# Performance work log

Measured on AMD Instinct MI355X. Metric: run time of the kernel, lower is better.

Reference implementation:

```python
import jax, jax.numpy as jnp
import numpy as np

N = 51200      # total nodes
E = 1638400    # total edges (avg degree 32)
G = 512        # graphs in batch
IN = 16        # input node features
H = 4          # heads
C = 32         # channels per head
HC = H * C     # 128, concat output width
SLOPE = 0.2    # LeakyReLU negative slope
BN_EPS = 1e-5


def _glorot(k, shape, fan):
    return jax.random.normal(k, shape, jnp.float32) / np.sqrt(fan).astype(np.float32)


def setup_inputs() -> dict:
    key = jax.random.key(0)
    ks = jax.random.split(key, 32)
    inp = {}
    inp['x'] = jax.random.normal(ks[0], (N, IN), jnp.float32)
    inp['edge_index'] = jax.random.randint(ks[1], (2, E), 0, N)
    inp['batch'] = jnp.sort(jax.random.randint(ks[2], (N,), 0, G))
    # GATv2 layer 1 (IN -> H*C)
    inp['l1_Wl'] = _glorot(ks[3], (IN, HC), IN)
    inp['l1_bl'] = jnp.zeros((HC,), jnp.float32)
    inp['l1_Wr'] = _glorot(ks[4], (IN, HC), IN)
    inp['l1_br'] = jnp.zeros((HC,), jnp.float32)
    inp['l1_att'] = _glorot(ks[5], (H, C), C)
    inp['l1_bias'] = jnp.zeros((HC,), jnp.float32)
    # GATv2 layer 2 (HC -> H*C)
    inp['l2_Wl'] = _glorot(ks[6], (HC, HC), HC)
    inp['l2_bl'] = jnp.zeros((HC,), jnp.float32)
    inp['l2_Wr'] = _glorot(ks[7], (HC, HC), HC)
    inp['l2_br'] = jnp.zeros((HC,), jnp.float32)
    inp['l2_att'] = _glorot(ks[8], (H, C), C)
    inp['l2_bias'] = jnp.zeros((HC,), jnp.float32)
    # MLP head (HC -> HC -> HC -> 2) with BatchNorm (eval mode, running stats 0/1)
    inp['fc1_W'] = _glorot(ks[9], (HC, HC), HC)
    inp['fc1_b'] = jnp.zeros((HC,), jnp.float32)
    inp['bn1_g'] = jnp.ones((HC,), jnp.float32)
    inp['bn1_b'] = jnp.zeros((HC,), jnp.float32)
    inp['fc2_W'] = _glorot(ks[10], (HC, HC), HC)
    inp['fc2_b'] = jnp.zeros((HC,), jnp.float32)
    inp['bn2_g'] = jnp.ones((HC,), jnp.float32)
    inp['bn2_b'] = jnp.zeros((HC,), jnp.float32)
    inp['fc3_W'] = _glorot(ks[11], (HC, 2), HC)
    inp['fc3_b'] = jnp.zeros((2,), jnp.float32)
    return inp


def gatv2_conv(x, src, dst, Wl, bl, Wr, br, att, bias):
    # PyG GATv2Conv (share_weights=False, concat=True), eval mode (no dropout).
    xl = (x @ Wl + bl).reshape(-1, H, C)  # source transform  [N,H,C]
    xr = (x @ Wr + br).reshape(-1, H, C)  # target transform  [N,H,C]
    e = jax.nn.leaky_relu(xl[src] + xr[dst], SLOPE)   # [E,H,C]
    score = jnp.einsum('ehc,hc->eh', e, att)          # [E,H]
    # segment softmax over edges sharing the same target node
    m = jax.ops.segment_max(score, dst, num_segments=N)
    ex = jnp.exp(score - m[dst])
    denom = jax.ops.segment_sum(ex, dst, num_segments=N)
    alpha = ex / (denom[dst] + 1e-16)                 # [E,H]
    out = jax.ops.segment_sum(xl[src] * alpha[:, :, None], dst, num_segments=N)
    return out.reshape(-1, HC) + bias


def reference(x, edge_index, batch,
              l1_Wl, l1_bl, l1_Wr, l1_br, l1_att, l1_bias,
              l2_Wl, l2_bl, l2_Wr, l2_br, l2_att, l2_bias,
              fc1_W, fc1_b, bn1_g, bn1_b,
              fc2_W, fc2_b, bn2_g, bn2_b,
              fc3_W, fc3_b):
    src, dst = edge_index[0], edge_index[1]
    h = jax.nn.relu(gatv2_conv(x, src, dst, l1_Wl, l1_bl, l1_Wr, l1_br, l1_att, l1_bias))
    h = jax.nn.relu(gatv2_conv(h, src, dst, l2_Wl, l2_bl, l2_Wr, l2_br, l2_att, l2_bias))
    # global mean pool over graphs
    s = jax.ops.segment_sum(h, batch, num_segments=G)
    cnt = jax.ops.segment_sum(jnp.ones((N,), h.dtype), batch, num_segments=G)
    g = s / jnp.maximum(cnt, 1.0)[:, None]            # [G,HC]
    # MLP head; BatchNorm1d in eval mode with running_mean=0, running_var=1
    def bn(z, gamma, beta):
        return z * (gamma / np.sqrt(1.0 + BN_EPS).astype(np.float32)) + beta
    g = jax.nn.relu(bn(g @ fc1_W + fc1_b, bn1_g, bn1_b))
    g = jax.nn.relu(bn(g @ fc2_W + fc2_b, bn2_g, bn2_b))
    return g @ fc3_W + fc3_b                          # [G,2]
```

## Files before the change

kernel.cpp:

```cpp
#include <hip/hip_runtime.h>
#include <math.h>

#define NN 51200
#define EE 1638400
#define GG 512
#define INF 16
#define HCC 128
#define NB 400
#define TILE 4096
#define NBLK (NN / 4)

typedef float vf2 __attribute__((ext_vector_type(2)));
#define FMA2 __builtin_elementwise_fma
#define MIN2 __builtin_elementwise_min
#define MAX2 __builtin_elementwise_max


__device__ __forceinline__ int wave_incl_scan(int v, int lane) {
#pragma unroll
    for (int d = 1; d < 64; d <<= 1) {
        int y = __shfl_up(v, d);
        if (lane >= d) v += y;
    }
    return v;
}

__global__ __launch_bounds__(256) void k_hist(const int* __restrict__ ei,
                                              int* __restrict__ bcnt) {
    __shared__ int h[NB];
    for (int i = threadIdx.x; i < NB; i += 256) h[i] = 0;
    __syncthreads();
    int e0 = blockIdx.x * TILE;
#pragma unroll
    for (int s = 0; s < 16; s++) {
        int d = ei[EE + e0 + s * 256 + threadIdx.x];
        atomicAdd(&h[d >> 7], 1);
    }
    __syncthreads();
    for (int i = threadIdx.x; i < NB; i += 256)
        if (h[i]) atomicAdd(&bcnt[i], h[i]);
}

__global__ __launch_bounds__(512) void k_scan2(const int* __restrict__ bcnt,
                                               int* __restrict__ bbase,
                                               int* __restrict__ gcur,
                                               int* __restrict__ rowptr) {
    __shared__ int sc[512];
    int t = threadIdx.x;
    int v = (t < NB) ? bcnt[t] : 0;
    sc[t] = v;
    __syncthreads();
    for (int off = 1; off < 512; off <<= 1) {
        int u = (t >= off) ? sc[t - off] : 0;
        __syncthreads();
        sc[t] += u;
        __syncthreads();
    }
    if (t < NB) { int ex = sc[t] - v; bbase[t] = ex; gcur[t] = ex; }
    if (t == 0) { bbase[NB] = EE; rowptr[NN] = EE; }
}

__global__ __launch_bounds__(512) void k_bin(const int* __restrict__ ei,
                                             int* __restrict__ gcur,
                                             unsigned* __restrict__ binned) {
    __shared__ int h[512];
    __shared__ int lexcl[NB], lcur[NB], baseg[NB];
    __shared__ unsigned stage[TILE];
    __shared__ int wsum[8];
    int t = threadIdx.x;
    int lane = t & 63, w = t >> 6;
    h[t] = 0;
    __syncthreads();
    int e0 = blockIdx.x * TILE;
    int sv[8], dv[8];
#pragma unroll
    for (int s = 0; s < 8; s++) {
        int e = e0 + s * 512 + t;
        sv[s] = ei[e];
        dv[s] = ei[EE + e];
        atomicAdd(&h[dv[s] >> 7], 1);
    }
    __syncthreads();
    int myh = h[t];
    int incl = wave_incl_scan(myh, lane);
    if (lane == 63) wsum[w] = incl;
    __syncthreads();
    int woff = 0;
    for (int i = 0; i < w; i++) woff += wsum[i];
    incl += woff;
    if (t < NB) {
        int ex = incl - myh;
        lexcl[t] = ex;
        lcur[t] = ex;
        baseg[t] = atomicAdd(&gcur[t], myh);
    }
    __syncthreads();
#pragma unroll
    for (int s = 0; s < 8; s++) {
        int b = dv[s] >> 7;
        int r = atomicAdd(&lcur[b], 1);
        stage[r] = (unsigned)sv[s] | ((unsigned)dv[s] << 16);
    }
    __syncthreads();
#pragma unroll
    for (int s = 0; s < 8; s++) {
        int idx = s * 512 + t;
        unsigned p = stage[idx];
        int b = (int)(p >> 23);
        binned[baseg[b] + idx - lexcl[b]] = p;
    }
}

__global__ __launch_bounds__(256) void k_csr(const unsigned* __restrict__ binned,
                                             const int* __restrict__ bbase,
                                             int* __restrict__ rowptr,
                                             int* __restrict__ col) {
    int b = blockIdx.x;
    int base = bbase[b];
    int cnt = bbase[b + 1] - base;
    __shared__ int nh[1024], ncur[1024];
    __shared__ int wsum[4];
    int t = threadIdx.x;
    int lane = t & 63, w = t >> 6;
#pragma unroll
    for (int i = 0; i < 4; i++) nh[t + 256 * i] = 0;
    __syncthreads();
    for (int e = t; e < cnt; e += 256) {
        unsigned p = binned[base + e];
        unsigned src = p & 0xFFFFu;
        int key = (int)(((p >> 16) & 127u) << 3) | (int)(src >> 13);
        atomicAdd(&nh[key], 1);
    }
    __syncthreads();
    int c0 = nh[4 * t + 0], c1 = nh[4 * t + 1], c2 = nh[4 * t + 2], c3 = nh[4 * t + 3];
    int tot = ((c0 + c1) + (c2 + c3));
    int incl = wave_incl_scan(tot, lane);
    if (lane == 63) wsum[w] = incl;
    __syncthreads();
    int woff = 0;
    for (int i = 0; i < w; i++) woff += wsum[i];
    int tex = incl + woff - tot;
    ncur[4 * t + 0] = base + tex;
    ncur[4 * t + 1] = base + tex + c0;
    ncur[4 * t + 2] = base + tex + c0 + c1;
    ncur[4 * t + 3] = base + tex + c0 + c1 + c2;
    if ((t & 1) == 0) rowptr[(b << 7) + (t >> 1)] = base + tex;
    __syncthreads();
    for (int e = t; e < cnt; e += 256) {
        unsigned p = binned[base + e];
        unsigned src = p & 0xFFFFu;
        int key = (int)(((p >> 16) & 127u) << 3) | (int)(src >> 13);
        int r = atomicAdd(&ncur[key], 1);
        col[r] = (int)src;
    }
}

__global__ __launch_bounds__(256) void k_lin1(const float* __restrict__ x,
                                              const float* __restrict__ Wl,
                                              const float* __restrict__ bl,
                                              const float* __restrict__ Wr,
                                              const float* __restrict__ br,
                                              float* __restrict__ xl,
                                              float* __restrict__ xr) {
    __shared__ float sx[2][INF];
    int j = threadIdx.x & 127;
    int ty = threadIdx.x >> 7;
    int row = blockIdx.x * 2 + ty;
    if (threadIdx.x < 32) {
        int r = blockIdx.x * 2 + (threadIdx.x >> 4);
        sx[threadIdx.x >> 4][threadIdx.x & 15] = x[(size_t)r * INF + (threadIdx.x & 15)];
    }
    __syncthreads();
    float al = bl[j], ar = br[j];
#pragma unroll
    for (int k = 0; k < INF; k++) {
        float xv = sx[ty][k];
        al = fmaf(xv, Wl[k * HCC + j], al);
        ar = fmaf(xv, Wr[k * HCC + j], ar);
    }
    size_t s = ((size_t)(j >> 5) * NN + row) * 32 + (j & 31);
    xl[s] = al;
    xr[s] = ar;
}

#define AST 129
#define BST 260
__global__ __launch_bounds__(512) void k_lin2(const float* __restrict__ hin,
                                              const float* __restrict__ Wl,
                                              const float* __restrict__ bl,
                                              const float* __restrict__ Wr,
                                              const float* __restrict__ br,
                                              float* __restrict__ outl,
                                              float* __restrict__ outr) {
    __shared__ float As[32 * AST];
    __shared__ float Bs[32 * BST];
    const int tid = threadIdx.x;
    const int cx = tid & 31;
    const int cy = tid >> 5;
    const int r0 = blockIdx.x * 128;

    float accL[8][4], accR[8][4];
#pragma unroll
    for (int j = 0; j < 8; j++)
#pragma unroll
        for (int i = 0; i < 4; i++) { accL[j][i] = 0.f; accR[j][i] = 0.f; }

    for (int k0 = 0; k0 < HCC; k0 += 32) {
#pragma unroll
        for (int s = 0; s < 2; s++) {
            int f = tid + 512 * s;
            int row = f >> 3;
            int kk = (f & 7) * 4;
            float4 v = *(const float4*)(hin + (size_t)(r0 + row) * HCC + k0 + kk);
            As[(kk + 0) * AST + row] = v.x;
            As[(kk + 1) * AST + row] = v.y;
            As[(kk + 2) * AST + row] = v.z;
            As[(kk + 3) * AST + row] = v.w;
        }
#pragma unroll
        for (int s = 0; s < 4; s++) {
            int g = tid + 512 * s;
            int kr = g >> 6;
            int c4 = g & 63;
            const float* srcp = (c4 < 32)
                ? (Wl + (size_t)(k0 + kr) * HCC + c4 * 4)
                : (Wr + (size_t)(k0 + kr) * HCC + (c4 - 32) * 4);
            *(float4*)&Bs[kr * BST + c4 * 4] = *(const float4*)srcp;
        }
        __syncthreads();
#pragma unroll 4
        for (int k = 0; k < 32; ++k) {
            float a[8];
#pragma unroll
            for (int j = 0; j < 8; ++j) a[j] = As[k * AST + cy + 16 * j];
            float4 b4l = *(const float4*)&Bs[k * BST + cx * 4];
            float4 b4r = *(const float4*)&Bs[k * BST + 128 + cx * 4];
#pragma unroll
            for (int j = 0; j < 8; ++j) {
                accL[j][0] = fmaf(a[j], b4l.x, accL[j][0]);
                accL[j][1] = fmaf(a[j], b4l.y, accL[j][1]);
                accL[j][2] = fmaf(a[j], b4l.z, accL[j][2]);
                accL[j][3] = fmaf(a[j], b4l.w, accL[j][3]);
                accR[j][0] = fmaf(a[j], b4r.x, accR[j][0]);
                accR[j][1] = fmaf(a[j], b4r.y, accR[j][1]);
                accR[j][2] = fmaf(a[j], b4r.z, accR[j][2]);
                accR[j][3] = fmaf(a[j], b4r.w, accR[j][3]);
            }
        }
        __syncthreads();
    }
    float4 bv_l = *(const float4*)(bl + cx * 4);
    float4 bv_r = *(const float4*)(br + cx * 4);
    const size_t plane = (size_t)(cx >> 3) * NN * 32;
    const int off = (cx & 7) * 4;
#pragma unroll
    for (int j = 0; j < 8; ++j) {
        int row = r0 + cy + 16 * j;
        float4 o;
        o.x = accL[j][0] + bv_l.x;
        o.y = accL[j][1] + bv_l.y;
        o.z = accL[j][2] + bv_l.z;
        o.w = accL[j][3] + bv_l.w;
        *(float4*)(outl + plane + (size_t)row * 32 + off) = o;
        o.x = accR[j][0] + bv_r.x;
        o.y = accR[j][1] + bv_r.y;
        o.z = accR[j][2] + bv_r.z;
        o.w = accR[j][3] + bv_r.w;
        *(float4*)(outr + plane + (size_t)row * 32 + off) = o;
    }
}

__global__ __launch_bounds__(256) void k_attn(const int* __restrict__ rowptr,
                                              const int* __restrict__ col,
                                              const float* __restrict__ xl,
                                              const float* __restrict__ xr,
                                              const float* __restrict__ att,
                                              const float* __restrict__ bias,
                                              float* __restrict__ hout) {
    const int wave = threadIdx.x >> 6;
    const int lane = threadIdx.x & 63;
    const int sub = lane >> 3;
    const int hl = (lane >> 2) & 1;
    const int hq = lane & 3;
    const int pair = blockIdx.x / NBLK;
    const int n = (blockIdx.x - pair * NBLK) * 4 + wave;
    const int head = 2 * pair + hl;

    const float* xlh = xl + (size_t)head * NN * 32;
    const float* xrp = xr + ((size_t)head * NN + n) * 32 + hq * 8;
    const float4 xrv0 = *(const float4*)(xrp);
    const float4 xrv1 = *(const float4*)(xrp + 4);
    const float4 at0 = *(const float4*)(att + head * 32 + hq * 8);
    const float4 at1 = *(const float4*)(att + head * 32 + hq * 8 + 4);
    const vf2 xr01 = {xrv0.x, xrv0.y}, xr23 = {xrv0.z, xrv0.w};
    const vf2 xr45 = {xrv1.x, xrv1.y}, xr67 = {xrv1.z, xrv1.w};
    const vf2 at01 = {at0.x, at0.y}, at23 = {at0.z, at0.w};
    const vf2 at45 = {at1.x, at1.y}, at67 = {at1.z, at1.w};
    const vf2 Z2 = {0.f, 0.f}, C2 = {0.2f, 0.2f};
    const unsigned choff = (unsigned)hq * 32u;

    const int base = rowptr[n];
    const int deg = rowptr[n + 1] - base;

    float m = -INFINITY, l = 0.f;
    vf2 a01 = Z2, a23 = Z2, a45 = Z2, a67 = Z2;

    for (int i0 = 0; i0 < deg; i0 += 64) {
        int mye = 0;
        if (i0 + lane < deg) mye = col[base + i0 + lane];
        const int cnt = min(64, deg - i0);
        const int events = (cnt + 15) >> 4;
        for (int g = 0; g < events; ++g) {
            float4 v0[2], v1[2];
            float p[2];
#pragma unroll
            for (int k = 0; k < 2; ++k) {
                const int src = __shfl(mye, 16 * g + 8 * k + sub);
                const unsigned voff = ((unsigned)src << 7) + choff;
                v0[k] = *(const float4*)((const char*)xlh + voff);
                v1[k] = *(const float4*)((const char*)xlh + voff + 16);
            }
#pragma unroll
            for (int k = 0; k < 2; ++k) {
                const vf2 v01 = {v0[k].x, v0[k].y}, v23 = {v0[k].z, v0[k].w};
                const vf2 v45 = {v1[k].x, v1[k].y}, v67 = {v1[k].z, v1[k].w};
                vf2 e, kk, p2;
                e = v01 + xr01; kk = FMA2(C2, MIN2(e, Z2), MAX2(e, Z2)); p2 = kk * at01;
                e = v23 + xr23; kk = FMA2(C2, MIN2(e, Z2), MAX2(e, Z2)); p2 = FMA2(kk, at23, p2);
                e = v45 + xr45; kk = FMA2(C2, MIN2(e, Z2), MAX2(e, Z2)); p2 = FMA2(kk, at45, p2);
                e = v67 + xr67; kk = FMA2(C2, MIN2(e, Z2), MAX2(e, Z2)); p2 = FMA2(kk, at67, p2);
                float pp = p2.x + p2.y;
                pp += __shfl_xor(pp, 1);
                pp += __shfl_xor(pp, 2);
                if ((16 * g + 8 * k + sub) >= cnt) pp = -INFINITY;
                p[k] = pp;
            }
            float pm = fmaxf(p[0], p[1]);
            pm = fmaxf(pm, __shfl_xor(pm, 8));
            pm = fmaxf(pm, __shfl_xor(pm, 16));
            pm = fmaxf(pm, __shfl_xor(pm, 32));
            const float mn = fmaxf(m, pm);
            const float sc = __expf(m - mn);
            const float w0 = __expf(p[0] - mn);
            const float w1 = __expf(p[1] - mn);
            l = fmaf(l, sc, w0 + w1);
            const vf2 S = {sc, sc}, W0 = {w0, w0}, W1 = {w1, w1};
            const vf2 u01 = {v0[0].x, v0[0].y}, u23 = {v0[0].z, v0[0].w};
            const vf2 u45 = {v1[0].x, v1[0].y}, u67 = {v1[0].z, v1[0].w};
            const vf2 t01 = {v0[1].x, v0[1].y}, t23 = {v0[1].z, v0[1].w};
            const vf2 t45 = {v1[1].x, v1[1].y}, t67 = {v1[1].z, v1[1].w};
            a01 = FMA2(W1, t01, FMA2(W0, u01, a01 * S));
            a23 = FMA2(W1, t23, FMA2(W0, u23, a23 * S));
            a45 = FMA2(W1, t45, FMA2(W0, u45, a45 * S));
            a67 = FMA2(W1, t67, FMA2(W0, u67, a67 * S));
            m = mn;
        }
    }
    l += __shfl_xor(l, 8);
    l += __shfl_xor(l, 16);
    l += __shfl_xor(l, 32);
    float af[8] = {a01.x, a01.y, a23.x, a23.y, a45.x, a45.y, a67.x, a67.y};
#pragma unroll
    for (int i = 0; i < 8; i++) {
        af[i] += __shfl_xor(af[i], 8);
        af[i] += __shfl_xor(af[i], 16);
        af[i] += __shfl_xor(af[i], 32);
    }
    const float inv = 1.f / (l + 1e-16f);
    if (sub == 0) {
        const float4 b0 = *(const float4*)(bias + head * 32 + hq * 8);
        const float4 b1 = *(const float4*)(bias + head * 32 + hq * 8 + 4);
        float4 o0, o1;
        o0.x = fmaxf(fmaf(af[0], inv, b0.x), 0.f);
        o0.y = fmaxf(fmaf(af[1], inv, b0.y), 0.f);
        o0.z = fmaxf(fmaf(af[2], inv, b0.z), 0.f);
        o0.w = fmaxf(fmaf(af[3], inv, b0.w), 0.f);
        o1.x = fmaxf(fmaf(af[4], inv, b1.x), 0.f);
        o1.y = fmaxf(fmaf(af[5], inv, b1.y), 0.f);
        o1.z = fmaxf(fmaf(af[6], inv, b1.z), 0.f);
        o1.w = fmaxf(fmaf(af[7], inv, b1.w), 0.f);
        float* hp = hout + (size_t)n * HCC + head * 32 + hq * 8;
        *(float4*)(hp) = o0;
        *(float4*)(hp + 4) = o1;
    }
}

__global__ __launch_bounds__(128) void k_head(const float* __restrict__ h,
                                              const int* __restrict__ batch,
                                              const float* __restrict__ fc1W, const float* __restrict__ fc1b,
                                              const float* __restrict__ bn1g, const float* __restrict__ bn1b,
                                              const float* __restrict__ fc2W, const float* __restrict__ fc2b,
                                              const float* __restrict__ bn2g, const float* __restrict__ bn2b,
                                              const float* __restrict__ fc3W, const float* __restrict__ fc3b,
                                              float* __restrict__ out) {
    int g = blockIdx.x;
    int j = threadIdx.x;
    __shared__ float buf[HCC], buf2[HCC];
    int lo = 0, hi = NN;
    while (lo < hi) { int mid = (lo + hi) >> 1; if (batch[mid] < g) lo = mid + 1; else hi = mid; }
    int s = lo;
    lo = 0; hi = NN;
    while (lo < hi) { int mid = (lo + hi) >> 1; if (batch[mid] < g + 1) lo = mid + 1; else hi = mid; }
    int e = lo;
    float s0 = 0.f, s1 = 0.f, s2 = 0.f, s3 = 0.f;
    int n = s;
    for (; n + 3 < e; n += 4) {
        s0 += h[(size_t)n * HCC + j];
        s1 += h[(size_t)(n + 1) * HCC + j];
        s2 += h[(size_t)(n + 2) * HCC + j];
        s3 += h[(size_t)(n + 3) * HCC + j];
    }
    for (; n < e; n++) s0 += h[(size_t)n * HCC + j];
    float sum = (s0 + s1) + (s2 + s3);
    float cnt = (float)(e - s);
    buf[j] = sum / fmaxf(cnt, 1.0f);
    __syncthreads();
    const float SQ = 1.00000499998749994f;
    float a = fc1b[j];
    for (int k = 0; k < HCC; k++) a = fmaf(buf[k], fc1W[k * HCC + j], a);
    a = fmaf(a, bn1g[j] / SQ, bn1b[j]);
    a = fmaxf(a, 0.f);
    buf2[j] = a;
    __syncthreads();
    a = fc2b[j];
    for (int k = 0; k < HCC; k++) a = fmaf(buf2[k], fc2W[k * HCC + j], a);
    a = fmaf(a, bn2g[j] / SQ, bn2b[j]);
    a = fmaxf(a, 0.f);
    buf[j] = a;
    __syncthreads();
    if (j < 2) {
        float o = fc3b[j];
        for (int k = 0; k < HCC; k++) o = fmaf(buf[k], fc3W[k * 2 + j], o);
        out[g * 2 + j] = o;
    }
}

extern "C" void kernel_launch(void* const* d_in, const int* in_sizes, int n_in,
                              void* d_out, int out_size, void* d_ws, size_t ws_size,
                              hipStream_t stream) {
    const float* x      = (const float*)d_in[0];
    const int*   ei     = (const int*)d_in[1];
    const int*   batch  = (const int*)d_in[2];
    const float* l1_Wl  = (const float*)d_in[3];
    const float* l1_bl  = (const float*)d_in[4];
    const float* l1_Wr  = (const float*)d_in[5];
    const float* l1_br  = (const float*)d_in[6];
    const float* l1_att = (const float*)d_in[7];
    const float* l1_bias= (const float*)d_in[8];
    const float* l2_Wl  = (const float*)d_in[9];
    const float* l2_bl  = (const float*)d_in[10];
    const float* l2_Wr  = (const float*)d_in[11];
    const float* l2_br  = (const float*)d_in[12];
    const float* l2_att = (const float*)d_in[13];
    const float* l2_bias= (const float*)d_in[14];
    const float* fc1_W  = (const float*)d_in[15];
    const float* fc1_b  = (const float*)d_in[16];
    const float* bn1_g  = (const float*)d_in[17];
    const float* bn1_b  = (const float*)d_in[18];
    const float* fc2_W  = (const float*)d_in[19];
    const float* fc2_b  = (const float*)d_in[20];
    const float* bn2_g  = (const float*)d_in[21];
    const float* bn2_b  = (const float*)d_in[22];
    const float* fc3_W  = (const float*)d_in[23];
    const float* fc3_b  = (const float*)d_in[24];
    float* out = (float*)d_out;

    float* xl = (float*)d_ws;
    float* xr = xl + (size_t)NN * HCC;
    float* h  = xr + (size_t)NN * HCC;
    int* rowptr = (int*)(h + (size_t)NN * HCC);
    int* col    = rowptr + (NN + 1);
    int* bcnt   = col + EE;
    int* bbase  = bcnt + NB;
    int* gcur   = bbase + (NB + 1);
    unsigned* binned = (unsigned*)xl;

    hipMemsetAsync(bcnt, 0, NB * sizeof(int), stream);
    k_hist<<<EE / TILE, 256, 0, stream>>>(ei, bcnt);
    k_scan2<<<1, 512, 0, stream>>>(bcnt, bbase, gcur, rowptr);
    k_bin<<<EE / TILE, 512, 0, stream>>>(ei, gcur, binned);
    k_csr<<<NB, 256, 0, stream>>>(binned, bbase, rowptr, col);

    k_lin1<<<NN / 2, 256, 0, stream>>>(x, l1_Wl, l1_bl, l1_Wr, l1_br, xl, xr);
    k_attn<<<2 * NBLK, 256, 0, stream>>>(rowptr, col, xl, xr, l1_att, l1_bias, h);

    k_lin2<<<NN / 128, 512, 0, stream>>>(h, l2_Wl, l2_bl, l2_Wr, l2_br, xl, xr);
    k_attn<<<2 * NBLK, 256, 0, stream>>>(rowptr, col, xl, xr, l2_att, l2_bias, h);

    k_head<<<GG, 128, 0, stream>>>(h, batch, fc1_W, fc1_b, bn1_g, bn1_b,
                                   fc2_W, fc2_b, bn2_g, bn2_b, fc3_W, fc3_b, out);
}
```

Baseline: 471.5 us.

## Drop shared-memory staging in layer-2 linear, read operands directly from global

Replaces the LDS-tiled GEMM in the layer-2 linear transform with a register-only loop that loads weight rows and input rows straight from global memory, four k at a time. This removes the shared-memory stores, barriers and LDS traffic. In exchange it relies on L1/L2 caching for reuse of the weights and of the input rows, since each input row is now read by 32 lanes. The uncoalesced per-thread input loads may cost more global bandwidth.

After: 499.1 us. 5.9% more time.

```diff
diff --git a/kernel.cpp b/kernel.cpp
--- a/kernel.cpp
+++ b/kernel.cpp
@@ -183,8 +183,6 @@
     xr[s] = ar;
 }
 
-#define AST 129
-#define BST 260
 __global__ __launch_bounds__(512) void k_lin2(const float* __restrict__ hin,
                                               const float* __restrict__ Wl,
                                               const float* __restrict__ bl,
@@ -192,8 +190,6 @@
                                               const float* __restrict__ br,
                                               float* __restrict__ outl,
                                               float* __restrict__ outr) {
-    __shared__ float As[32 * AST];
-    __shared__ float Bs[32 * BST];
     const int tid = threadIdx.x;
     const int cx = tid & 31;
     const int cy = tid >> 5;
@@ -205,49 +201,30 @@
 #pragma unroll
         for (int i = 0; i < 4; i++) { accL[j][i] = 0.f; accR[j][i] = 0.f; }
 
-    for (int k0 = 0; k0 < HCC; k0 += 32) {
-#pragma unroll
-        for (int s = 0; s < 2; s++) {
-            int f = tid + 512 * s;
-            int row = f >> 3;
-            int kk = (f & 7) * 4;
-            float4 v = *(const float4*)(hin + (size_t)(r0 + row) * HCC + k0 + kk);
-            As[(kk + 0) * AST + row] = v.x;
-            As[(kk + 1) * AST + row] = v.y;
-            As[(kk + 2) * AST + row] = v.z;
-            As[(kk + 3) * AST + row] = v.w;
+    const float* ap = hin + (size_t)(r0 + cy) * HCC;
+
+    for (int k0 = 0; k0 < HCC; k0 += 4) {
+        float4 bL[4], bR[4];
+#pragma unroll
+        for (int kk = 0; kk < 4; kk++) {
+            bL[kk] = *(const float4*)(Wl + (size_t)(k0 + kk) * HCC + cx * 4);
+            bR[kk] = *(const float4*)(Wr + (size_t)(k0 + kk) * HCC + cx * 4);
         }
 #pragma unroll
-        for (int s = 0; s < 4; s++) {
-            int g = tid + 512 * s;
-            int kr = g >> 6;
-            int c4 = g & 63;
-            const float* srcp = (c4 < 32)
-                ? (Wl + (size_t)(k0 + kr) * HCC + c4 * 4)
-                : (Wr + (size_t)(k0 + kr) * HCC + (c4 - 32) * 4);
-            *(float4*)&Bs[kr * BST + c4 * 4] = *(const float4*)srcp;
-        }
-        __syncthreads();
-#pragma unroll 4
-        for (int k = 0; k < 32; ++k) {
-            float a[8];
-#pragma unroll
-            for (int j = 0; j < 8; ++j) a[j] = As[k * AST + cy + 16 * j];
-            float4 b4l = *(const float4*)&Bs[k * BST + cx * 4];
-            float4 b4r = *(const float4*)&Bs[k * BST + 128 + cx * 4];
-#pragma unroll
-            for (int j = 0; j < 8; ++j) {
-                accL[j][0] = fmaf(a[j], b4l.x, accL[j][0]);
-                accL[j][1] = fmaf(a[j], b4l.y, accL[j][1]);
-                accL[j][2] = fmaf(a[j], b4l.z, accL[j][2]);
-                accL[j][3] = fmaf(a[j], b4l.w, accL[j][3]);
-                accR[j][0] = fmaf(a[j], b4r.x, accR[j][0]);
-                accR[j][1] = fmaf(a[j], b4r.y, accR[j][1]);
-                accR[j][2] = fmaf(a[j], b4r.z, accR[j][2]);
-                accR[j][3] = fmaf(a[j], b4r.w, accR[j][3]);
+        for (int j = 0; j < 8; j++) {
+            const float4 a = *(const float4*)(ap + (size_t)(16 * j) * HCC + k0);
+#pragma unroll
+            for (int i = 0; i < 4; i++) {
+                accL[j][i] = fmaf(a.x, ((const float*)&bL[0])[i], accL[j][i]);
+                accL[j][i] = fmaf(a.y, ((const float*)&bL[1])[i], accL[j][i]);
+                accL[j][i] = fmaf(a.z, ((const float*)&bL[2])[i], accL[j][i]);
+                accL[j][i] = fmaf(a.w, ((const float*)&bL[3])[i], accL[j][i]);
+                accR[j][i] = fmaf(a.x, ((const float*)&bR[0])[i], accR[j][i]);
+                accR[j][i] = fmaf(a.y, ((const float*)&bR[1])[i], accR[j][i]);
+                accR[j][i] = fmaf(a.z, ((const float*)&bR[2])[i], accR[j][i]);
+                accR[j][i] = fmaf(a.w, ((const float*)&bR[3])[i], accR[j][i]);
             }
         }
-        __syncthreads();
     }
     float4 bv_l = *(const float4*)(bl + cx * 4);
     float4 bv_r = *(const float4*)(br + cx * 4);
```
